# Optimization experiments

Measured on AMD Instinct MI355X. Metric: run time of the kernel, lower is better.

## Reference

```python
import jax, jax.numpy as jnp
import numpy as np

L = 64      # system size
H = 64      # hiddenSize
IN = 4      # inputDim (POVM)
B = 4096    # batch of configurations


def _make_w(k, din, dout):
    # Padded block-triangular weight: W[idx, i, j, s] is nonzero only for j >= idx,
    # matching Dense(features=(L-idx)*dout) output scattered into rows idx: of h.
    W = jax.random.normal(k, (L, din, L, dout), dtype=jnp.float32) / jnp.sqrt(jnp.float32(din))
    mask = (jnp.arange(L)[:, None] <= jnp.arange(L)[None, :]).astype(jnp.float32)  # [idx, j]
    return W * mask[:, None, :, None]


def setup_inputs() -> dict:
    key = jax.random.key(0)
    ks = jax.random.split(key, 7)
    x = jax.random.randint(ks[0], (B, L), 0, IN, dtype=jnp.int32)
    W0 = _make_w(ks[1], IN, H)
    W1 = _make_w(ks[2], H, H)
    W2 = _make_w(ks[3], H, 4)
    # bias exists only for site idx==0; its (L*size,) output reshaped to (L, size)
    # is added to all rows of h, so it acts as the initial value of h[d].
    b0 = 0.1 * jax.random.normal(ks[4], (L, H), dtype=jnp.float32)
    b1 = 0.1 * jax.random.normal(ks[5], (L, H), dtype=jnp.float32)
    b2 = 0.1 * jax.random.normal(ks[6], (L, 4), dtype=jnp.float32)
    return {"x": x, "W0": W0, "W1": W1, "W2": W2, "b0": b0, "b1": b1, "b2": b2}


def reference(x, W0, W1, W2, b0, b1, b2):
    Bn = x.shape[0]
    x_oh = jax.nn.one_hot(x, IN, dtype=jnp.float32)                      # (B, L, 4)
    # ffn_cell input: one-hot of x[:-1], shifted right with a zero row prepended
    x_in = jnp.concatenate([jnp.zeros((Bn, 1, IN), jnp.float32), x_oh[:, :-1]], axis=1)

    h0 = jnp.broadcast_to(b0, (Bn, L, H))
    h1 = jnp.broadcast_to(b1, (Bn, L, H))
    h2 = jnp.broadcast_to(b2, (Bn, L, 4))

    def step(carry, inp):
        h0, h1, h2 = carry
        a, idx, w0, w1, w2 = inp                                        # a: (B, 4)
        h0 = h0 + jnp.einsum('bi,ijs->bjs', a, w0)                      # scatter-add rows >= idx
        a = jax.nn.elu(jnp.take(h0, idx, axis=1))                       # (B, H)
        h1 = h1 + jnp.einsum('bi,ijs->bjs', a, w1)
        a = jax.nn.elu(jnp.take(h1, idx, axis=1))
        h2 = h2 + jnp.einsum('bi,ijs->bjs', a, w2)
        return (h0, h1, h2), None

    xs = (jnp.swapaxes(x_in, 0, 1), jnp.arange(L), W0, W1, W2)
    (h0, h1, h2), _ = jax.lax.scan(step, (h0, h1, h2), xs)

    out = jax.nn.elu(h2)                                                # (B, L, 4)
    logp = jnp.sum(jax.nn.log_softmax(out, axis=-1) * x_oh, axis=(1, 2))
    return logp                                                         # (B,)
```

## Files before the change

### kernel.cpp

```cpp
#include <hip/hip_runtime.h>
#include <hip/hip_bf16.h>

#define LL 64
#define HH 64
#define KDIM 4096

typedef __attribute__((ext_vector_type(8))) short bf16x8;
typedef __attribute__((ext_vector_type(4))) short s16x4;
typedef __attribute__((ext_vector_type(4))) float f32x4;

__device__ inline short f2bf(float f) {
    __hip_bfloat16 h = __float2bfloat16(f);
    return *reinterpret_cast<short*>(&h);
}
__device__ inline float elu1(float x) { return x > 0.f ? x : expm1f(x); }

__device__ inline void global_load_lds16(const short* g, short* l) {
    __builtin_amdgcn_global_load_lds(
        (const __attribute__((address_space(1))) unsigned int*)g,
        (__attribute__((address_space(3))) unsigned int*)l,
        16, 0, 0);
}

__global__ __launch_bounds__(256) void k_prep_all(
    const float* __restrict__ W1, short* __restrict__ W1T,
    const float* __restrict__ W2, short* __restrict__ W2T,
    const float* __restrict__ W0, short* __restrict__ W0T,
    const int* __restrict__ x, short* __restrict__ Xoh)
{
    int bid = blockIdx.x;
    if (bid >= 18432) {
        int id = bid - 18432;
        int b = id * 4 + (threadIdx.x >> 6);
        int t = threadIdx.x & 63;
        s16x4 v = {0, 0, 0, 0};
        if (t > 0) {
            int xi = x[b * LL + t - 1];
            v[xi] = (short)0x3F80;
        }
        *(s16x4*)(Xoh + (size_t)b * 256 + t * 4) = v;
        return;
    }
    const float* in; short* out; int R, C, bx, by;
    if (bid < 16384) {
        bx = bid & 127; by = bid >> 7;
        if (by * 32 >= bx * 32 + 160) return;
        in = W1; out = W1T; R = 4096; C = 4096;
    } else if (bid < 17408) {
        int id = bid - 16384; bx = id & 7; by = id >> 3;
        in = W2; out = W2T; R = 4096; C = 256;
    } else {
        int id = bid - 17408; bx = id & 127; by = id >> 7;
        in = W0; out = W0T; R = 256; C = 4096;
    }
    __shared__ float tile[32][33];
    int tx = threadIdx.x & 31, ty = threadIdx.x >> 5;
    size_t r0 = (size_t)by * 32, c0 = (size_t)bx * 32;
#pragma unroll
    for (int i = 0; i < 32; i += 8)
        tile[ty + i][tx] = in[(r0 + ty + i) * C + (c0 + tx)];
    __syncthreads();
#pragma unroll
    for (int i = 0; i < 32; i += 8)
        out[(c0 + ty + i) * R + (r0 + tx)] = f2bf(tile[tx][ty + i]);
}

template<int SHIFT, bool OUT_BF16>
__global__ __launch_bounds__(256) void k_gemm_bt64_db(
    const short* __restrict__ A, const short* __restrict__ BT,
    const float* __restrict__ bias, void* __restrict__ Cv,
    int M, int N, int K)
{
    constexpr int BM = 128, BN = 128, BK = 64;
    constexpr int BUF = BM * BK;
    __shared__ short As[2 * BUF];
    __shared__ short Bs[2 * BUF];

    int m0 = blockIdx.x * BM;
    int n0 = ((int)gridDim.y - 1 - (int)blockIdx.y) * BN;
    int tid = threadIdx.x;
    int wave = tid >> 6, lane = tid & 63;
    int wm = (wave >> 1) * 64, wn = (wave & 1) * 64;

    int ke;
    if constexpr (SHIFT >= 0) ke = (n0 + BN) << SHIFT;
    else                      ke = (n0 + BN) >> (-SHIFT);
    int k_end = min(K, ke);
    int nt = (k_end + BK - 1) / BK;

    f32x4 acc[4][4] = {};

    const short* gA[4]; const short* gB[4];
    int lofs[4];
#pragma unroll
    for (int c = 0; c < 4; ++c) {
        int r  = (wave * 4 + c) * 8 + (lane >> 3);
        int gc = (((lane & 7) - r) & 7) * 8;
        gA[c] = A  + (size_t)(m0 + r) * K + gc;
        gB[c] = BT + (size_t)(n0 + r) * K + gc;
        lofs[c] = (wave * 4 + c) * 512;
    }

    int q = lane >> 4, lrow = lane & 15;
    int offA[4][2], offB[4][2];
#pragma unroll
    for (int i = 0; i < 4; ++i) {
#pragma unroll
        for (int h = 0; h < 2; ++h) {
            int ra = wm + i * 16 + lrow;
            int rb = wn + i * 16 + lrow;
            offA[i][h] = ra * 64 + ((h * 4 + q + ra) & 7) * 8;
            offB[i][h] = rb * 64 + ((h * 4 + q + rb) & 7) * 8;
        }
    }

#pragma unroll
    for (int c = 0; c < 4; ++c) {
        global_load_lds16(gA[c], As + lofs[c]);
        global_load_lds16(gB[c], Bs + lofs[c]);
    }
    asm volatile("s_waitcnt vmcnt(0)" ::: "memory");
    __builtin_amdgcn_s_barrier();
    asm volatile("" ::: "memory");

    int cur = 0;
    for (int t = 0; t < nt; ++t) {
        if (t + 1 < nt) {
            int kb = (t + 1) * BK;
            int bo = (cur ^ 1) * BUF;
#pragma unroll
            for (int c = 0; c < 4; ++c) {
                global_load_lds16(gA[c] + kb, As + bo + lofs[c]);
                global_load_lds16(gB[c] + kb, Bs + bo + lofs[c]);
            }
        }
        const short* bA = As + cur * BUF;
        const short* bB = Bs + cur * BUF;
        __builtin_amdgcn_s_setprio(1);
#pragma unroll
        for (int h = 0; h < 2; ++h) {
            bf16x8 af[4], bfr[4];
#pragma unroll
            for (int i = 0; i < 4; ++i) {
                af[i]  = *(const bf16x8*)(bA + offA[i][h]);
                bfr[i] = *(const bf16x8*)(bB + offB[i][h]);
            }
#pragma unroll
            for (int mi = 0; mi < 4; ++mi)
#pragma unroll
                for (int ni = 0; ni < 4; ++ni)
                    acc[mi][ni] = __builtin_amdgcn_mfma_f32_16x16x32_bf16(
                        af[mi], bfr[ni], acc[mi][ni], 0, 0, 0);
        }
        __builtin_amdgcn_s_setprio(0);
        asm volatile("s_waitcnt vmcnt(0)" ::: "memory");
        __builtin_amdgcn_s_barrier();
        asm volatile("" ::: "memory");
        cur ^= 1;
    }

    int lcol = lane & 15;
    int lr4  = (lane >> 4) * 4;
#pragma unroll
    for (int mi = 0; mi < 4; ++mi) {
#pragma unroll
        for (int ni = 0; ni < 4; ++ni) {
            int col = n0 + wn + ni * 16 + lcol;
            float bv = bias[col];
#pragma unroll
            for (int r = 0; r < 4; ++r) {
                int row = m0 + wm + mi * 16 + lr4 + r;
                float v = elu1(acc[mi][ni][r] + bv);
                if (OUT_BF16) ((short*)Cv)[(size_t)row * N + col] = f2bf(v);
                else          ((float*)Cv)[(size_t)row * N + col] = v;
            }
        }
    }
}

template<int SHIFT, int ZSPLIT>
__global__ __launch_bounds__(256) void k_gemm_bt64_splitk(
    const short* __restrict__ A, const short* __restrict__ BT,
    float* __restrict__ part, int M, int N, int K)
{
    constexpr int BM = 128, BN = 128, BK = 64;
    __shared__ short As[BM * BK];
    __shared__ short Bs[BN * BK];

    int m0 = blockIdx.x * BM;
    int n0 = ((int)gridDim.y - 1 - (int)blockIdx.y) * BN;
    int z = blockIdx.z;
    int tid = threadIdx.x;
    int wave = tid >> 6, lane = tid & 63;
    int wm = (wave >> 1) * 64, wn = (wave & 1) * 64;

    int k_end = min(K, (n0 + BN) << SHIFT);
    int chunk = ((k_end / ZSPLIT + BK - 1) / BK) * BK;
    int kb0 = z * chunk;
    int kb1 = min(k_end, kb0 + chunk);

    f32x4 acc[4][4] = {};

    const short* gA[4]; const short* gB[4];
    short* lAs[4]; short* lBs[4];
#pragma unroll
    for (int c = 0; c < 4; ++c) {
        int r  = (wave * 4 + c) * 8 + (lane >> 3);
        int gc = (((lane & 7) - r) & 7) * 8;
        gA[c] = A  + (size_t)(m0 + r) * K + gc;
        gB[c] = BT + (size_t)(n0 + r) * K + gc;
        lAs[c] = As + (wave * 4 + c) * 512;
        lBs[c] = Bs + (wave * 4 + c) * 512;
    }

    int q = lane >> 4, lrow = lane & 15;
    int offA[4][2], offB[4][2];
#pragma unroll
    for (int i = 0; i < 4; ++i) {
#pragma unroll
        for (int h = 0; h < 2; ++h) {
            int ra = wm + i * 16 + lrow;
            int rb = wn + i * 16 + lrow;
            offA[i][h] = ra * 64 + ((h * 4 + q + ra) & 7) * 8;
            offB[i][h] = rb * 64 + ((h * 4 + q + rb) & 7) * 8;
        }
    }

    for (int kb = kb0; kb < kb1; kb += BK) {
        __syncthreads();
#pragma unroll
        for (int c = 0; c < 4; ++c) {
            global_load_lds16(gA[c] + kb, lAs[c]);
            global_load_lds16(gB[c] + kb, lBs[c]);
        }
        __syncthreads();

#pragma unroll
        for (int h = 0; h < 2; ++h) {
            bf16x8 af[4], bfr[4];
#pragma unroll
            for (int i = 0; i < 4; ++i) {
                af[i]  = *(const bf16x8*)(As + offA[i][h]);
                bfr[i] = *(const bf16x8*)(Bs + offB[i][h]);
            }
#pragma unroll
            for (int mi = 0; mi < 4; ++mi)
#pragma unroll
                for (int ni = 0; ni < 4; ++ni)
                    acc[mi][ni] = __builtin_amdgcn_mfma_f32_16x16x32_bf16(
                        af[mi], bfr[ni], acc[mi][ni], 0, 0, 0);
        }
    }

    float* p = part + (size_t)z * M * N;
    int lcol = lane & 15;
    int lr4  = (lane >> 4) * 4;
#pragma unroll
    for (int mi = 0; mi < 4; ++mi)
#pragma unroll
        for (int ni = 0; ni < 4; ++ni) {
            int col = n0 + wn + ni * 16 + lcol;
#pragma unroll
            for (int r = 0; r < 4; ++r) {
                int row = m0 + wm + mi * 16 + lr4 + r;
                p[(size_t)row * N + col] = acc[mi][ni][r];
            }
        }
}

__global__ __launch_bounds__(256) void k_logp_fused(
    const float* __restrict__ part, const float* __restrict__ b2,
    const int* __restrict__ x, float* __restrict__ logp)
{
    const size_t MN = (size_t)4096 * 256;
    int b = blockIdx.x * 4 + (threadIdx.x >> 6);
    int j = threadIdx.x & 63;
    size_t idx = (size_t)b * 256 + j * 4;

    f32x4 o = *(const f32x4*)(part + idx);
#pragma unroll
    for (int z = 1; z < 8; ++z) {
        f32x4 p = *(const f32x4*)(part + idx + (size_t)z * MN);
#pragma unroll
        for (int s = 0; s < 4; ++s) o[s] += p[s];
    }
    f32x4 bv = *(const f32x4*)(b2 + j * 4);
#pragma unroll
    for (int s = 0; s < 4; ++s)
        o[s] = elu1(o[s] + bv[s]);

    float m = fmaxf(fmaxf(o[0], o[1]), fmaxf(o[2], o[3]));
    float lse = m + logf(expf(o[0] - m) + expf(o[1] - m) +
                         expf(o[2] - m) + expf(o[3] - m));
    int xi = x[b * LL + j];
    float sel = (xi == 0) ? o[0] : (xi == 1) ? o[1] : (xi == 2) ? o[2] : o[3];
    float c = sel - lse;
#pragma unroll
    for (int off = 32; off > 0; off >>= 1)
        c += __shfl_down(c, off, 64);
    if (j == 0) logp[b] = c;
}

extern "C" void kernel_launch(void* const* d_in, const int* in_sizes, int n_in,
                              void* d_out, int out_size, void* d_ws, size_t ws_size,
                              hipStream_t stream)
{
    const int*   x  = (const int*)  d_in[0];
    const float* W0 = (const float*)d_in[1];
    const float* W1 = (const float*)d_in[2];
    const float* W2 = (const float*)d_in[3];
    const float* b0 = (const float*)d_in[4];
    const float* b1 = (const float*)d_in[5];
    const float* b2 = (const float*)d_in[6];
    float* logp = (float*)d_out;

    char* ws = (char*)d_ws;
    short* W1T  = (short*)(ws);
    short* W2T  = (short*)(ws + (size_t)33554432);
    short* W0T  = (short*)(ws + (size_t)35651584);
    short* Xoh  = (short*)(ws + (size_t)37748736);
    short* A1   = (short*)(ws + (size_t)39845888);
    float* part = (float*)(ws + (size_t)39845888);
    short* A2   = (short*)(ws + (size_t)73400320);

    k_prep_all<<<19456, 256, 0, stream>>>(W1, W1T, W2, W2T, W0, W0T, x, Xoh);

    k_gemm_bt64_db<-4, true><<<dim3(32, 32), 256, 0, stream>>>(Xoh, W0T, b0, A1, 4096, 4096, 256);

    k_gemm_bt64_db<0, true><<<dim3(32, 32), 256, 0, stream>>>(A1, W1T, b1, A2, 4096, 4096, 4096);

    k_gemm_bt64_splitk<4, 8><<<dim3(32, 2, 8), 256, 0, stream>>>(A2, W2T, part, 4096, 256, 4096);

    k_logp_fused<<<1024, 256, 0, stream>>>(part, b2, x, logp);
}
```

Measured before the change: 150.1 us.

## Overlap next-tile loads with compute via partial vmcnt waits and double-buffer split-K GEMM

```diff
diff --git a/kernel.cpp b/kernel.cpp
--- a/kernel.cpp
+++ b/kernel.cpp
@@ -66,7 +66,7 @@
 }
 
 template<int SHIFT, bool OUT_BF16>
-__global__ __launch_bounds__(256) void k_gemm_bt64_db(
+__global__ __launch_bounds__(256) void k_gemm_bt64_pipe(
     const short* __restrict__ A, const short* __restrict__ BT,
     const float* __restrict__ bias, void* __restrict__ Cv,
     int M, int N, int K)
@@ -119,9 +119,6 @@
         global_load_lds16(gA[c], As + lofs[c]);
         global_load_lds16(gB[c], Bs + lofs[c]);
     }
-    asm volatile("s_waitcnt vmcnt(0)" ::: "memory");
-    __builtin_amdgcn_s_barrier();
-    asm volatile("" ::: "memory");
 
     int cur = 0;
     for (int t = 0; t < nt; ++t) {
@@ -133,7 +130,13 @@
                 global_load_lds16(gA[c] + kb, As + bo + lofs[c]);
                 global_load_lds16(gB[c] + kb, Bs + bo + lofs[c]);
             }
-        }
+            asm volatile("s_waitcnt vmcnt(8)" ::: "memory");
+        } else {
+            asm volatile("s_waitcnt vmcnt(0)" ::: "memory");
+        }
+        __builtin_amdgcn_s_barrier();
+        asm volatile("" ::: "memory");
+
         const short* bA = As + cur * BUF;
         const short* bB = Bs + cur * BUF;
         __builtin_amdgcn_s_setprio(1);
@@ -153,7 +156,7 @@
                         af[mi], bfr[ni], acc[mi][ni], 0, 0, 0);
         }
         __builtin_amdgcn_s_setprio(0);
-        asm volatile("s_waitcnt vmcnt(0)" ::: "memory");
+        asm volatile("" ::: "memory");
         __builtin_amdgcn_s_barrier();
         asm volatile("" ::: "memory");
         cur ^= 1;
@@ -184,8 +187,9 @@
     float* __restrict__ part, int M, int N, int K)
 {
     constexpr int BM = 128, BN = 128, BK = 64;
-    __shared__ short As[BM * BK];
-    __shared__ short Bs[BN * BK];
+    constexpr int BUF = BM * BK;
+    __shared__ short As[2 * BUF];
+    __shared__ short Bs[2 * BUF];
 
     int m0 = blockIdx.x * BM;
     int n0 = ((int)gridDim.y - 1 - (int)blockIdx.y) * BN;
@@ -198,19 +202,19 @@
     int chunk = ((k_end / ZSPLIT + BK - 1) / BK) * BK;
     int kb0 = z * chunk;
     int kb1 = min(k_end, kb0 + chunk);
+    int nt = (kb1 - kb0 + BK - 1) / BK;
 
     f32x4 acc[4][4] = {};
 
     const short* gA[4]; const short* gB[4];
-    short* lAs[4]; short* lBs[4];
+    int lofs[4];
 #pragma unroll
     for (int c = 0; c < 4; ++c) {
         int r  = (wave * 4 + c) * 8 + (lane >> 3);
         int gc = (((lane & 7) - r) & 7) * 8;
-        gA[c] = A  + (size_t)(m0 + r) * K + gc;
-        gB[c] = BT + (size_t)(n0 + r) * K + gc;
-        lAs[c] = As + (wave * 4 + c) * 512;
-        lBs[c] = Bs + (wave * 4 + c) * 512;
+        gA[c] = A  + (size_t)(m0 + r) * K + gc + kb0;
+        gB[c] = BT + (size_t)(n0 + r) * K + gc + kb0;
+        lofs[c] = (wave * 4 + c) * 512;
     }
 
     int q = lane >> 4, lrow = lane & 15;
@@ -226,22 +230,53 @@
         }
     }
 
-    for (int kb = kb0; kb < kb1; kb += BK) {
-        __syncthreads();
-#pragma unroll
-        for (int c = 0; c < 4; ++c) {
-            global_load_lds16(gA[c] + kb, lAs[c]);
-            global_load_lds16(gB[c] + kb, lBs[c]);
-        }
-        __syncthreads();
-
+    if (nt <= 0) {
+        int lcol = lane & 15, lr4 = (lane >> 4) * 4;
+        float* p = part + (size_t)z * M * N;
+#pragma unroll
+        for (int mi = 0; mi < 4; ++mi)
+#pragma unroll
+            for (int ni = 0; ni < 4; ++ni)
+#pragma unroll
+                for (int r = 0; r < 4; ++r)
+                    p[(size_t)(m0 + wm + mi * 16 + lr4 + r) * N
+                      + (n0 + wn + ni * 16 + lcol)] = 0.f;
+        return;
+    }
+
+#pragma unroll
+    for (int c = 0; c < 4; ++c) {
+        global_load_lds16(gA[c], As + lofs[c]);
+        global_load_lds16(gB[c], Bs + lofs[c]);
+    }
+
+    int cur = 0;
+    for (int t = 0; t < nt; ++t) {
+        if (t + 1 < nt) {
+            int kb = (t + 1) * BK;
+            int bo = (cur ^ 1) * BUF;
+#pragma unroll
+            for (int c = 0; c < 4; ++c) {
+                global_load_lds16(gA[c] + kb, As + bo + lofs[c]);
+                global_load_lds16(gB[c] + kb, Bs + bo + lofs[c]);
+            }
+            asm volatile("s_waitcnt vmcnt(8)" ::: "memory");
+        } else {
+            asm volatile("s_waitcnt vmcnt(0)" ::: "memory");
+        }
+        __builtin_amdgcn_s_barrier();
+        asm volatile("" ::: "memory");
+
+        const short* bA = As + cur * BUF;
+        const short* bB = Bs + cur * BUF;
+        __builtin_amdgcn_s_setprio(1);
 #pragma unroll
         for (int h = 0; h < 2; ++h) {
             bf16x8 af[4], bfr[4];
 #pragma unroll
             for (int i = 0; i < 4; ++i) {
-                af[i]  = *(const bf16x8*)(As + offA[i][h]);
-                bfr[i] = *(const bf16x8*)(Bs + offB[i][h]);
+                af[i]  = *(const bf16x8*)(bA + offA[i][h]);
+                bfr[i] = *(const bf16x8*)(bB + offB[i][h]);
             }
 #pragma unroll
             for (int mi = 0; mi < 4; ++mi)
@@ -250,6 +285,11 @@
                     acc[mi][ni] = __builtin_amdgcn_mfma_f32_16x16x32_bf16(
                         af[mi], bfr[ni], acc[mi][ni], 0, 0, 0);
         }
+        __builtin_amdgcn_s_setprio(0);
+        asm volatile("" ::: "memory");
+        __builtin_amdgcn_s_barrier();
+        asm volatile("" ::: "memory");
+        cur ^= 1;
     }
 
     float* p = part + (size_t)z * M * N;
@@ -325,9 +365,9 @@
 
     k_prep_all<<<19456, 256, 0, stream>>>(W1, W1T, W2, W2T, W0, W0T, x, Xoh);
 
-    k_gemm_bt64_db<-4, true><<<dim3(32, 32), 256, 0, stream>>>(Xoh, W0T, b0, A1, 4096, 4096, 256);
-
-    k_gemm_bt64_db<0, true><<<dim3(32, 32), 256, 0, stream>>>(A1, W1T, b1, A2, 4096, 4096, 4096);
+    k_gemm_bt64_pipe<-4, true><<<dim3(32, 32), 256, 0, stream>>>(Xoh, W0T, b0, A1, 4096, 4096, 256);
+
+    k_gemm_bt64_pipe<0, true><<<dim3(32, 32), 256, 0, stream>>>(A1, W1T, b1, A2, 4096, 4096, 4096);
 
     k_gemm_bt64_splitk<4, 8><<<dim3(32, 2, 8), 256, 0, stream>>>(A2, W2T, part, 4096, 256, 4096);
 
```

Result: no change. 147.2 us (-1.9%).
